# Performance work log

Measured on AMD Instinct MI355X. Metric: run time of the kernel, lower is better.

Reference implementation:

```python
import jax, jax.numpy as jnp
import numpy as np

W_BITS = 8       # default precision = max(precisions)
MIN_PREC = 4     # min(precisions)
GROUP_SIZE = 128


def make_new_byte_indices(total_bytes: int) -> np.ndarray:
    # Replicates make_new_byte_indices_torch. Note: in the torch code,
    # argsort(argsort(new_idx)) == new_idx (it is a permutation), so the
    # "unpermute" is a gather with new_idx itself.
    bytes_per_thread = 4
    threads_per_warp = 32
    bytes_per_warp = threads_per_warp * bytes_per_thread  # 128
    full = total_bytes // bytes_per_warp * bytes_per_warp
    rem = total_bytes - full
    parts = []
    if full > 0:
        bi = np.arange(full)
        warp_offsets = (bi // bytes_per_warp) * bytes_per_warp
        thread_indices = bi % threads_per_warp
        byte_off = ((bi % bytes_per_warp) // threads_per_warp) ^ 3
        parts.append(warp_offsets + thread_indices * bytes_per_thread + byte_off)
    if rem > 0:
        ri = np.arange(rem)
        adj = rem // bytes_per_thread
        if adj > 0:
            warp_offsets = (ri // bytes_per_warp) * bytes_per_warp
            thread_indices = ri % adj
            byte_off = (ri // adj) ^ 3
            parts.append(warp_offsets + thread_indices * 4 + byte_off + full)
        else:
            parts.append(np.arange(full, full + rem))
    return np.concatenate(parts).astype(np.int64)


def dequant(qweight, scale, zero, w_bits=W_BITS):
    _, N, in_chunks = qweight.shape
    total_bytes = in_chunks * 4
    in_features = in_chunks * 32
    q = qweight[:w_bits]
    # little-endian byte view of int32 (matches torch .view(torch.uint8))
    b = jnp.stack([(q >> (8 * k)) & 0xFF for k in range(4)], axis=-1)
    b = b.reshape(w_bits, N, total_bytes)  # int32 values in [0,255]
    idx = jnp.asarray(make_new_byte_indices(total_bytes))
    b = b[:, :, idx]
    # unpack bits, MSB first within each byte
    bits = jnp.stack([(b >> i) & 1 for i in reversed(range(8))], axis=-1)
    bits = bits.reshape(w_bits, N, in_features)  # [w_bits, N, in_features]
    plane_w = jnp.asarray([1 << (w_bits - 1 - k) for k in range(w_bits)], dtype=jnp.int32)
    qw = jnp.einsum('b,bni->ni', plane_w, bits)  # int32 in [0, 2^w_bits-1]
    weight_f = qw.astype(jnp.float32)
    bit_err = w_bits - MIN_PREC
    zero = zero * (2.0 ** bit_err)
    scale_pc = jnp.repeat(scale, GROUP_SIZE, axis=1)[:, :in_features]
    zero_pc = jnp.repeat(zero, GROUP_SIZE, axis=1)[:, :in_features]
    return scale_pc * (weight_f - zero_pc)  # [N, in_features]


def setup_inputs() -> dict:
    key = jax.random.key(0)
    kx, kq, ks, kz, kb = jax.random.split(key, 5)
    B, S, IN, OUT, G = 4, 2048, 4096, 4096, GROUP_SIZE
    x = jax.random.normal(kx, (B, S, IN), dtype=jnp.float32)
    qweight = jax.random.randint(kq, (8, OUT, IN // 32), 0, 2147483647, dtype=jnp.int32)
    scale = jax.random.uniform(ks, (OUT, IN // G), dtype=jnp.float32) * 0.01 + 1e-4
    zero = jax.random.uniform(kz, (OUT, IN // G), dtype=jnp.float32) * 8.0
    bias = jax.random.normal(kb, (OUT,), dtype=jnp.float32)
    return {"x": x, "qweight": qweight, "scale": scale, "zero": zero, "bias": bias}


def reference(x, qweight, scale, zero, bias):
    weight = dequant(qweight, scale, zero, W_BITS)  # [out, in]
    return jnp.matmul(x, weight.T) + bias
```

## Files before the change

### kernel.cpp

```cpp
#include <hip/hip_runtime.h>
#include <hip/hip_bf16.h>
#include <stdint.h>

typedef __attribute__((ext_vector_type(8))) short short8;
typedef __attribute__((ext_vector_type(4))) float f32x4;

#define M_DIM 8192
#define N_DIM 4096
#define K_DIM 4096
#define BM 256
#define BN 256
#define BK 64

static __device__ __forceinline__ unsigned short f32_to_bf16(float f) {
  union { float f; unsigned int u; } v; v.f = f;
  unsigned int u = v.u;
  u += 0x7fffu + ((u >> 16) & 1u);
  return (unsigned short)(u >> 16);
}

__global__ void cast_x_kernel(const float* __restrict__ x,
                              unsigned short* __restrict__ xb) {
  size_t i = ((size_t)blockIdx.x * blockDim.x + threadIdx.x) * 8;
  if (i >= (size_t)M_DIM * K_DIM) return;
  float4 v0 = *reinterpret_cast<const float4*>(x + i);
  float4 v1 = *reinterpret_cast<const float4*>(x + i + 4);
  short8 o;
  o[0] = (short)f32_to_bf16(v0.x);
  o[1] = (short)f32_to_bf16(v0.y);
  o[2] = (short)f32_to_bf16(v0.z);
  o[3] = (short)f32_to_bf16(v0.w);
  o[4] = (short)f32_to_bf16(v1.x);
  o[5] = (short)f32_to_bf16(v1.y);
  o[6] = (short)f32_to_bf16(v1.z);
  o[7] = (short)f32_to_bf16(v1.w);
  *reinterpret_cast<short8*>(xb + i) = o;
}

__global__ void dequant_kernel(const int* __restrict__ qw,
                               const float* __restrict__ scale,
                               const float* __restrict__ zero,
                               unsigned short* __restrict__ W) {
  int idx = blockIdx.x * blockDim.x + threadIdx.x;
  if (idx >= N_DIM * 128) return;
  int n = idx >> 7;
  int c = idx & 127;
  unsigned int w[8];
#pragma unroll
  for (int k = 0; k < 8; ++k)
    w[k] = (unsigned int)qw[(size_t)k * (N_DIM * 128) + idx];
  int wp = c >> 5, t = c & 31;
#pragma unroll
  for (int s = 0; s < 4; ++s) {
    int r = s ^ 3;
    unsigned int by[8];
#pragma unroll
    for (int k = 0; k < 8; ++k) by[k] = (w[k] >> (8 * r)) & 0xffu;
    int ibase = wp * 1024 + s * 256 + t * 8;
    int g = ibase >> 7;
    float sc = scale[n * 32 + g];
    float zp = zero[n * 32 + g] * 16.0f;
    short8 o;
#pragma unroll
    for (int u = 0; u < 8; ++u) {
      unsigned int q = 0;
#pragma unroll
      for (int k = 0; k < 8; ++k)
        q |= ((by[k] >> (7 - u)) & 1u) << (7 - k);
      o[u] = (short)f32_to_bf16(sc * ((float)q - zp));
    }
    *reinterpret_cast<short8*>(&W[(size_t)n * K_DIM + ibase]) = o;
  }
}


#define VMCNT2 asm volatile("s_waitcnt vmcnt(2)" ::: "memory")
#define VMCNT0 asm volatile("s_waitcnt vmcnt(0)" ::: "memory")
#define NOOP ((void)0)

#define STG(G, GROWB, KT, LDSC) do {                                           \
  const unsigned short* sb_ = (G) + ((size_t)(GROWB) * K_DIM + (KT) * 64);     \
  __builtin_amdgcn_global_load_lds(                                            \
      (const __attribute__((address_space(1))) void*)(sb_ + s_off0),           \
      (__attribute__((address_space(3))) void*)(smem + (LDSC) + wslot),        \
      16, 0, 0);                                                               \
  __builtin_amdgcn_global_load_lds(                                            \
      (const __attribute__((address_space(1))) void*)(sb_ + s_off1),           \
      (__attribute__((address_space(3))) void*)(smem + (LDSC) + 8192 + wslot), \
      16, 0, 0);                                                               \
} while (0)
#define STG_A(BUF, H, KT) STG(Ag, m0 + (H)*128, (KT), ((BUF)*2 + (H)) * 16384)
#define STG_B(BUF, H, KT) STG(Bg, n0 + (H)*128, (KT), 65536 + ((BUF)*2 + (H)) * 16384)

#define LA(BUF, QM, KK) do {                                                   \
  _Pragma("unroll") for (int mf_ = 0; mf_ < 4; ++mf_)                          \
    a_[mf_][KK] = *(const short8*)(smem + ((KK) ? a_off1 : a_off0) +           \
        (((BUF)*2 + (QM)) * 16384 + mf_ * 2048));                              \
} while (0)
#define LB(BUF, QN, KK) do {                                                   \
  _Pragma("unroll") for (int nf_ = 0; nf_ < 2; ++nf_)                          \
    b_[nf_][KK] = *(const short8*)(smem + ((KK) ? b_off1 : b_off0) +           \
        (((BUF)*2 + (QN)) * 16384 + nf_ * 2048));                              \
} while (0)

#define MFMA_KK(QM, QN, KK)                                                    \
  _Pragma("unroll") for (int mf_ = 0; mf_ < 4; ++mf_)                          \
    _Pragma("unroll") for (int nf_ = 0; nf_ < 2; ++nf_)                        \
      acc[QM][QN][mf_][nf_] = __builtin_amdgcn_mfma_f32_16x16x32_bf16(         \
          a_[mf_][KK], b_[nf_][KK], acc[QM][QN][mf_][nf_], 0, 0, 0)

#define REGION(QM, QN, RD0, RD1, STAGE, WAITV) do {                            \
  __builtin_amdgcn_s_barrier();                                                \
  WAITV;                                                                       \
  asm volatile("s_waitcnt lgkmcnt(0)" ::: "memory");                           \
  __builtin_amdgcn_sched_barrier(0);                                           \
  __builtin_amdgcn_s_setprio(1);                                               \
  STAGE;                                                                       \
  MFMA_KK(QM, QN, 0);                                                          \
  RD0;                                                                         \
  __builtin_amdgcn_sched_barrier(0);                                           \
  MFMA_KK(QM, QN, 1);                                                          \
  RD1;                                                                         \
  __builtin_amdgcn_s_setprio(0);                                               \
} while (0)

__global__ __launch_bounds__(512, 2) void gemm_kernel(
    const unsigned short* __restrict__ Ag,
    const unsigned short* __restrict__ Bg,
    const float* __restrict__ bias,
    float* __restrict__ C) {
  __shared__ __align__(16) char smem[131072];

  int bid = blockIdx.x;
  int cpx = gridDim.x >> 3;
  int swz = (bid & 7) * cpx + (bid >> 3);
  int tm = swz >> 4;
  int tn = swz & 15;
  int m0 = tm * BM, n0 = tn * BN;

  int tid = threadIdx.x;
  int lane = tid & 63;
  int wid = tid >> 6;
  int wr = wid >> 2, wc = wid & 3;

  const int xorv = (lane & 7) << 4;
  const int hi4 = (lane >> 4) << 4;
  const int wrbase = wr * 64 + (lane & 15);
  const int wcbase = wc * 32 + (lane & 15);
  const int a_off0 = (wrbase << 7) + (hi4 ^ xorv);
  const int a_off1 = (wrbase << 7) + ((64 | hi4) ^ xorv);
  const int b_off0 = 65536 + (wcbase << 7) + (hi4 ^ xorv);
  const int b_off1 = 65536 + (wcbase << 7) + ((64 | hi4) ^ xorv);
  const int wslot = (tid >> 6) << 10;
  const int s_lr0 = tid >> 3, s_lr1 = 64 + (tid >> 3);
  const int s_off0 = s_lr0 * K_DIM + (((tid & 7) ^ (s_lr0 & 7)) << 3);
  const int s_off1 = s_lr1 * K_DIM + (((tid & 7) ^ (s_lr1 & 7)) << 3);

  short8 a_[4][2], b_[2][2];
  f32x4 acc[2][2][4][2];
#pragma unroll
  for (int i = 0; i < 2; ++i)
#pragma unroll
    for (int j = 0; j < 2; ++j)
#pragma unroll
      for (int mf = 0; mf < 4; ++mf)
#pragma unroll
        for (int nf = 0; nf < 2; ++nf) acc[i][j][mf][nf] = (f32x4){0.f, 0.f, 0.f, 0.f};

  STG_B(0, 0, 0); STG_A(0, 0, 0); STG_B(0, 1, 0); STG_A(0, 1, 0);
  STG_A(1, 0, 1);
  VMCNT2;
  __builtin_amdgcn_s_barrier();
  LA(0, 0, 0); LB(0, 0, 0); LA(0, 0, 1); LB(0, 0, 1);

  for (int t = 0; t < 31; ++t) {
    const int kt1 = 2 * t + 1;
    REGION(0, 0, LB(0,1,0),            LB(0,1,1),            STG_B(1,0,kt1),   VMCNT2);
    REGION(0, 1, LA(0,1,0),            LA(0,1,1),            STG_B(1,1,kt1),   VMCNT2);
    REGION(1, 1, LB(0,0,0),            LB(0,0,1),            STG_A(1,1,kt1),   VMCNT2);
    REGION(1, 0, LA(1,0,0); LB(1,0,0), LA(1,0,1); LB(1,0,1), STG_B(0,0,kt1+1), VMCNT2);
    REGION(0, 0, LB(1,1,0),            LB(1,1,1),            STG_A(0,0,kt1+1), VMCNT2);
    REGION(0, 1, LA(1,1,0),            LA(1,1,1),            STG_B(0,1,kt1+1), VMCNT2);
    REGION(1, 1, LB(1,0,0),            LB(1,0,1),            STG_A(0,1,kt1+1), VMCNT2);
    REGION(1, 0, LA(0,0,0); LB(0,0,0), LA(0,0,1); LB(0,0,1), STG_A(1,0,kt1+2), VMCNT2);
  }
  REGION(0, 0, LB(0,1,0),            LB(0,1,1),            STG_B(1,0,63), VMCNT2);
  REGION(0, 1, LA(0,1,0),            LA(0,1,1),            STG_B(1,1,63), VMCNT2);
  REGION(1, 1, LB(0,0,0),            LB(0,0,1),            STG_A(1,1,63), VMCNT2);
  REGION(1, 0, LA(1,0,0); LB(1,0,0), LA(1,0,1); LB(1,0,1), NOOP,          VMCNT2);
  REGION(0, 0, LB(1,1,0),            LB(1,1,1),            NOOP,          VMCNT0);
  REGION(0, 1, LA(1,1,0),            LA(1,1,1),            NOOP,          NOOP);
  REGION(1, 1, LB(1,0,0),            LB(1,0,1),            NOOP,          NOOP);
  REGION(1, 0, NOOP,                 NOOP,                 NOOP,          NOOP);

#pragma unroll
  for (int qn = 0; qn < 2; ++qn)
#pragma unroll
    for (int nf = 0; nf < 2; ++nf) {
      int gcol = n0 + qn * 128 + wc * 32 + nf * 16 + (lane & 15);
      float bv = bias[gcol];
#pragma unroll
      for (int qm = 0; qm < 2; ++qm)
#pragma unroll
        for (int mf = 0; mf < 4; ++mf) {
          int grow = m0 + qm * 128 + wr * 64 + mf * 16 + ((lane >> 4) << 2);
          f32x4 v = acc[qm][qn][mf][nf];
#pragma unroll
          for (int j = 0; j < 4; ++j)
            C[(size_t)(grow + j) * N_DIM + gcol] = v[j] + bv;
        }
    }
}

extern "C" void kernel_launch(void* const* d_in, const int* in_sizes, int n_in,
                              void* d_out, int out_size, void* d_ws, size_t ws_size,
                              hipStream_t stream) {
  const float* x       = (const float*)d_in[0];
  const int*   qweight = (const int*)d_in[1];
  const float* scale   = (const float*)d_in[2];
  const float* zero    = (const float*)d_in[3];
  const float* bias    = (const float*)d_in[4];
  float* out = (float*)d_out;

  unsigned short* Xb = (unsigned short*)d_ws;
  unsigned short* Wb = Xb + (size_t)M_DIM * K_DIM;

  cast_x_kernel<<<(M_DIM * K_DIM / 8) / 256, 256, 0, stream>>>(x, Xb);
  dequant_kernel<<<(N_DIM * 128) / 256, 256, 0, stream>>>(qweight, scale, zero, Wb);
  gemm_kernel<<<(M_DIM / BM) * (N_DIM / BN), 512, 0, stream>>>(Xb, Wb, bias, out);
}
```

Measured before the change: 263.0 us.

## Double-buffer A/B fragment registers to issue LDS reads ahead of MFMAs

```diff
diff --git a/kernel.cpp b/kernel.cpp
--- a/kernel.cpp
+++ b/kernel.cpp
@@ -92,35 +92,35 @@
 #define STG_A(BUF, H, KT) STG(Ag, m0 + (H)*128, (KT), ((BUF)*2 + (H)) * 16384)
 #define STG_B(BUF, H, KT) STG(Bg, n0 + (H)*128, (KT), 65536 + ((BUF)*2 + (H)) * 16384)
 
-#define LA(BUF, QM, KK) do {                                                   \
+#define LA_K(SET, BUF, QM, KK) do {                                            \
   _Pragma("unroll") for (int mf_ = 0; mf_ < 4; ++mf_)                          \
-    a_[mf_][KK] = *(const short8*)(smem + ((KK) ? a_off1 : a_off0) +           \
+    SET[mf_][KK] = *(const short8*)(smem + ((KK) ? a_off1 : a_off0) +          \
         (((BUF)*2 + (QM)) * 16384 + mf_ * 2048));                              \
 } while (0)
-#define LB(BUF, QN, KK) do {                                                   \
-  _Pragma("unroll") for (int nf_ = 0; nf_ < 2; ++nf_)                          \
-    b_[nf_][KK] = *(const short8*)(smem + ((KK) ? b_off1 : b_off0) +           \
+#define LA_ALL(SET, BUF, QM) do { LA_K(SET, BUF, QM, 0); LA_K(SET, BUF, QM, 1); } while (0)
+#define LB_ALL(SET, BUF, QN) do {                                              \
+  _Pragma("unroll") for (int nf_ = 0; nf_ < 2; ++nf_) {                        \
+    SET[nf_][0] = *(const short8*)(smem + b_off0 +                             \
         (((BUF)*2 + (QN)) * 16384 + nf_ * 2048));                              \
-} while (0)
-
-#define MFMA_KK(QM, QN, KK)                                                    \
-  _Pragma("unroll") for (int mf_ = 0; mf_ < 4; ++mf_)                          \
-    _Pragma("unroll") for (int nf_ = 0; nf_ < 2; ++nf_)                        \
-      acc[QM][QN][mf_][nf_] = __builtin_amdgcn_mfma_f32_16x16x32_bf16(         \
-          a_[mf_][KK], b_[nf_][KK], acc[QM][QN][mf_][nf_], 0, 0, 0)
-
-#define REGION(QM, QN, RD0, RD1, STAGE, WAITV) do {                            \
+    SET[nf_][1] = *(const short8*)(smem + b_off1 +                             \
+        (((BUF)*2 + (QN)) * 16384 + nf_ * 2048));                              \
+  } } while (0)
+
+#define REGION(QM, QN, AS, BS, EARLY, STAGE, LATE, WAITV) do {                 \
   __builtin_amdgcn_s_barrier();                                                \
   WAITV;                                                                       \
   asm volatile("s_waitcnt lgkmcnt(0)" ::: "memory");                           \
   __builtin_amdgcn_sched_barrier(0);                                           \
   __builtin_amdgcn_s_setprio(1);                                               \
   STAGE;                                                                       \
-  MFMA_KK(QM, QN, 0);                                                          \
-  RD0;                                                                         \
+  EARLY;                                                                       \
   __builtin_amdgcn_sched_barrier(0);                                           \
-  MFMA_KK(QM, QN, 1);                                                          \
-  RD1;                                                                         \
+  _Pragma("unroll") for (int mf_ = 0; mf_ < 4; ++mf_)                          \
+    _Pragma("unroll") for (int nf_ = 0; nf_ < 2; ++nf_)                        \
+      _Pragma("unroll") for (int kk_ = 0; kk_ < 2; ++kk_)                      \
+        acc[QM][QN][mf_][nf_] = __builtin_amdgcn_mfma_f32_16x16x32_bf16(       \
+            AS[mf_][kk_], BS[nf_][kk_], acc[QM][QN][mf_][nf_], 0, 0, 0);       \
+  LATE;                                                                        \
   __builtin_amdgcn_s_setprio(0);                                               \
 } while (0)
 
@@ -156,7 +156,7 @@
   const int s_off0 = s_lr0 * K_DIM + (((tid & 7) ^ (s_lr0 & 7)) << 3);
   const int s_off1 = s_lr1 * K_DIM + (((tid & 7) ^ (s_lr1 & 7)) << 3);
 
-  short8 a_[4][2], b_[2][2];
+  short8 a0_[4][2], a1_[4][2], b0_[2][2], b1_[2][2];
   f32x4 acc[2][2][4][2];
 #pragma unroll
   for (int i = 0; i < 2; ++i)
@@ -171,27 +171,27 @@
   STG_A(1, 0, 1);
   VMCNT2;
   __builtin_amdgcn_s_barrier();
-  LA(0, 0, 0); LB(0, 0, 0); LA(0, 0, 1); LB(0, 0, 1);
+  LA_ALL(a0_, 0, 0); LB_ALL(b0_, 0, 0);
 
   for (int t = 0; t < 31; ++t) {
     const int kt1 = 2 * t + 1;
-    REGION(0, 0, LB(0,1,0),            LB(0,1,1),            STG_B(1,0,kt1),   VMCNT2);
-    REGION(0, 1, LA(0,1,0),            LA(0,1,1),            STG_B(1,1,kt1),   VMCNT2);
-    REGION(1, 1, LB(0,0,0),            LB(0,0,1),            STG_A(1,1,kt1),   VMCNT2);
-    REGION(1, 0, LA(1,0,0); LB(1,0,0), LA(1,0,1); LB(1,0,1), STG_B(0,0,kt1+1), VMCNT2);
-    REGION(0, 0, LB(1,1,0),            LB(1,1,1),            STG_A(0,0,kt1+1), VMCNT2);
-    REGION(0, 1, LA(1,1,0),            LA(1,1,1),            STG_B(0,1,kt1+1), VMCNT2);
-    REGION(1, 1, LB(1,0,0),            LB(1,0,1),            STG_A(0,1,kt1+1), VMCNT2);
-    REGION(1, 0, LA(0,0,0); LB(0,0,0), LA(0,0,1); LB(0,0,1), STG_A(1,0,kt1+2), VMCNT2);
+    REGION(0,0, a0_,b0_, LB_ALL(b1_,0,1),  STG_B(1,0,kt1),   NOOP,            VMCNT2);
+    REGION(0,1, a0_,b1_, LA_ALL(a1_,0,1),  STG_B(1,1,kt1),   NOOP,            VMCNT2);
+    REGION(1,1, a1_,b1_, LA_K(a0_,1,0,0),  STG_A(1,1,kt1),   NOOP,            VMCNT2);
+    REGION(1,0, a1_,b0_, LA_K(a0_,1,0,1),  STG_B(0,0,kt1+1), LB_ALL(b0_,1,0), VMCNT2);
+    REGION(0,0, a0_,b0_, LB_ALL(b1_,1,1),  STG_A(0,0,kt1+1), NOOP,            VMCNT2);
+    REGION(0,1, a0_,b1_, LA_ALL(a1_,1,1),  STG_B(0,1,kt1+1), NOOP,            VMCNT2);
+    REGION(1,1, a1_,b1_, NOOP,             STG_A(0,1,kt1+1), NOOP,            VMCNT2);
+    REGION(1,0, a1_,b0_, LA_ALL(a0_,0,0),  STG_A(1,0,kt1+2), LB_ALL(b0_,0,0), VMCNT2);
   }
-  REGION(0, 0, LB(0,1,0),            LB(0,1,1),            STG_B(1,0,63), VMCNT2);
-  REGION(0, 1, LA(0,1,0),            LA(0,1,1),            STG_B(1,1,63), VMCNT2);
-  REGION(1, 1, LB(0,0,0),            LB(0,0,1),            STG_A(1,1,63), VMCNT2);
-  REGION(1, 0, LA(1,0,0); LB(1,0,0), LA(1,0,1); LB(1,0,1), NOOP,          VMCNT2);
-  REGION(0, 0, LB(1,1,0),            LB(1,1,1),            NOOP,          VMCNT0);
-  REGION(0, 1, LA(1,1,0),            LA(1,1,1),            NOOP,          NOOP);
-  REGION(1, 1, LB(1,0,0),            LB(1,0,1),            NOOP,          NOOP);
-  REGION(1, 0, NOOP,                 NOOP,                 NOOP,          NOOP);
+  REGION(0,0, a0_,b0_, LB_ALL(b1_,0,1),  STG_B(1,0,63), NOOP,            VMCNT2);
+  REGION(0,1, a0_,b1_, LA_ALL(a1_,0,1),  STG_B(1,1,63), NOOP,            VMCNT2);
+  REGION(1,1, a1_,b1_, LA_K(a0_,1,0,0),  STG_A(1,1,63), NOOP,            VMCNT2);
+  REGION(1,0, a1_,b0_, LA_K(a0_,1,0,1),  NOOP,          LB_ALL(b0_,1,0), VMCNT2);
+  REGION(0,0, a0_,b0_, LB_ALL(b1_,1,1),  NOOP,          NOOP,            VMCNT0);
+  REGION(0,1, a0_,b1_, LA_ALL(a1_,1,1),  NOOP,          NOOP,            NOOP);
+  REGION(1,1, a1_,b1_, NOOP,             NOOP,          NOOP,            NOOP);
+  REGION(1,0, a1_,b0_, NOOP,             NOOP,          NOOP,            NOOP);
 
 #pragma unroll
   for (int qn = 0; qn < 2; ++qn)
```

After: 274.9 us. +4.5%, slower.
